# Performance work log

Hardware: AMD Instinct MI355X
Metric: run time of the kernel (lower is better)

The kernel has to match this reference:

```python
import jax, jax.numpy as jnp
import numpy as np

HEAD_NUM = 8
ATT_DIM = 64
NUM_UNITS = HEAD_NUM * ATT_DIM  # 512
B, T, D = 8, 1024, NUM_UNITS
NEG_BIG = -2.0**32 + 1.0


def _sinusoidal_table(max_len, num_hidden):
    P = np.zeros((1, max_len, num_hidden), dtype=np.float32)
    X = np.arange(max_len, dtype=np.float32).reshape(-1, 1) / np.power(
        10000.0, np.arange(0, num_hidden, 2, dtype=np.float32) / num_hidden)
    P[:, :, 0::2] = np.sin(X)
    P[:, :, 1::2] = np.cos(X)
    return P


def setup_inputs() -> dict:
    key = jax.random.key(0)
    ks = jax.random.split(key, 8)
    w_scale = 0.02
    return {
        "queries": jax.random.normal(ks[0], (B, T, D), dtype=jnp.float32),
        "keys": jax.random.normal(ks[1], (B, T, D), dtype=jnp.float32),
        "query_masks": jnp.ones((B, T), dtype=jnp.float32),
        "key_masks": jnp.ones((B, T), dtype=jnp.float32),
        "pos_table": jnp.asarray(_sinusoidal_table(T, D)),
        "W_Query": jax.random.normal(ks[2], (D, D), dtype=jnp.float32) * w_scale,
        "W_key": jax.random.normal(ks[3], (D, D), dtype=jnp.float32) * w_scale,
        "W_Value": jax.random.normal(ks[4], (D, D), dtype=jnp.float32) * w_scale,
        "fw1": jax.random.normal(ks[5], (D, 4 * D), dtype=jnp.float32) * w_scale,
        "fw2": jax.random.normal(ks[6], (4 * D, D), dtype=jnp.float32) * w_scale,
    }


def reference(queries, keys, query_masks, key_masks, pos_table,
              W_Query, W_key, W_Value, fw1, fw2):
    h, dh = HEAD_NUM, ATT_DIM
    pe_scale = jnp.asarray(NUM_UNITS ** 0.5, dtype=queries.dtype)
    pos = pos_table[:, :queries.shape[1], :] * pe_scale  # scale=True
    q_in = queries + pos
    k_in = keys + pos

    q = jnp.einsum('btd,de->bte', q_in, W_Query)
    k = jnp.einsum('btd,de->bte', k_in, W_key)
    # Faithful to source: values computed from the projected keys.
    v = jnp.einsum('btd,de->bte', k, W_Value)

    # split heads: (B,T,h*dh) -> (h,B,T,dh)
    def heads(x):
        return x.reshape(B, T, h, dh).transpose(2, 0, 1, 3)
    qh, kh, vh = heads(q), heads(k), heads(v)

    scores = jnp.einsum('hbqd,hbkd->hbqk', qh, kh) / (dh ** 0.5)
    # key padding mask
    scores = jnp.where(key_masks[None, :, None, :] == 1.0, scores, NEG_BIG)
    # blinding: mask the diagonal
    eye = jnp.eye(T, dtype=bool)
    scores = jnp.where(eye[None, None, :, :], NEG_BIG, scores)
    attn = jax.nn.softmax(scores, axis=-1)
    attn = attn * query_masks[None, :, :, None]

    out = jnp.einsum('hbqk,hbkd->hbqd', attn, vh)
    result = out.transpose(1, 2, 0, 3).reshape(B, T, D)  # merge heads

    result = result + q_in  # residual (use_res, queries after PE)

    # feed-forward with residual
    hidden = jax.nn.relu(jnp.einsum('btd,df->btf', result, fw1))
    ffn = jnp.einsum('btf,fd->btd', hidden, fw2)
    result = result + ffn

    # output_type == 'mean'
    return jnp.mean(result, axis=1, keepdims=True)  # (B,1,D)
```

## Files before the change

kernel.cpp:

```cpp
#include <hip/hip_runtime.h>


typedef __bf16 bf16x8 __attribute__((ext_vector_type(8)));
typedef __bf16 bf16x4 __attribute__((ext_vector_type(4)));
typedef float f32x4 __attribute__((ext_vector_type(4)));
typedef unsigned short u16x8 __attribute__((ext_vector_type(8)));
typedef unsigned short u16x4 __attribute__((ext_vector_type(4)));

#define MFMA_BF16(a, b, c) __builtin_amdgcn_mfma_f32_16x16x32_bf16((a), (b), (c), 0, 0, 0)
#define NEGBIG (-4294967295.0f)

#define GLL16(g, l)                                                                 \
    __builtin_amdgcn_global_load_lds((__attribute__((address_space(1))) void*)(g),  \
                                     (__attribute__((address_space(3))) void*)(l),  \
                                     16, 0, 0)

static __device__ __forceinline__ unsigned short f2bf(float f) {
    __bf16 h = (__bf16)f;
    return __builtin_bit_cast(unsigned short, h);
}
static __device__ __forceinline__ float bf2f(unsigned short h) {
    return __builtin_bit_cast(float, ((unsigned int)h) << 16);
}

__global__ __launch_bounds__(256) void prep_kernel(
    const float* __restrict__ q, const float* __restrict__ k,
    const float* __restrict__ pos,
    unsigned short* __restrict__ qo, unsigned short* __restrict__ ko)
{
    size_t i = ((size_t)blockIdx.x * 256 + threadIdx.x) * 4;
    size_t td = i & (size_t)(1024 * 512 - 1);
    float4 qv = *(const float4*)(q + i);
    float4 kv = *(const float4*)(k + i);
    float4 pv = *(const float4*)(pos + td);
    const float S = 22.627416997969522f;
    u16x4 qr, kr;
    qr[0] = f2bf(qv.x + pv.x * S); qr[1] = f2bf(qv.y + pv.y * S);
    qr[2] = f2bf(qv.z + pv.z * S); qr[3] = f2bf(qv.w + pv.w * S);
    kr[0] = f2bf(kv.x + pv.x * S); kr[1] = f2bf(kv.y + pv.y * S);
    kr[2] = f2bf(kv.z + pv.z * S); kr[3] = f2bf(kv.w + pv.w * S);
    *(u16x4*)(qo + i) = qr;
    *(u16x4*)(ko + i) = kr;
}

__global__ __launch_bounds__(256) void wconv_kernel(
    const float* __restrict__ w0, const float* __restrict__ w1, const float* __restrict__ w2,
    const float* __restrict__ w3, const float* __restrict__ w4,
    unsigned short* __restrict__ o0, unsigned short* __restrict__ o1, unsigned short* __restrict__ o2,
    unsigned short* __restrict__ o3, unsigned short* __restrict__ o4,
    unsigned short* __restrict__ wkp)
{
    int id = blockIdx.x;
    const float* in; unsigned short* out; int K, N, kt, nt; bool dup = false;
    if (id < 768) {
        int m = id >> 8; id &= 255;
        in  = (m == 0) ? w0 : ((m == 1) ? w1 : w2);
        out = (m == 0) ? o0 : ((m == 1) ? o1 : o2);
        dup = (m == 1);
        K = 512; N = 512; kt = id >> 4; nt = id & 15;
    } else if (id < 1792) {
        id -= 768; in = w3; out = o3; K = 512; N = 2048; kt = id >> 6; nt = id & 63;
    } else {
        id -= 1792; in = w4; out = o4; K = 2048; N = 512; kt = id >> 4; nt = id & 15;
    }
    int k0 = kt * 32, n0 = nt * 32;
    __shared__ float tile[32][33];
    int tx = threadIdx.x & 31, ty = threadIdx.x >> 5;
#pragma unroll
    for (int i = 0; i < 32; i += 8) {
        float v = in[(size_t)(k0 + ty + i) * N + n0 + tx];
        tile[ty + i][tx] = v;
        if (dup) wkp[(size_t)(k0 + ty + i) * 512 + n0 + tx] = f2bf(v);
    }
    __syncthreads();
#pragma unroll
    for (int i = 0; i < 32; i += 8)
        out[(size_t)(n0 + ty + i) * K + k0 + tx] = f2bf(tile[tx][ty + i]);
}

static __device__ __forceinline__ void gemm_core(
    const unsigned short* __restrict__ A,
    const unsigned short* __restrict__ Bt,
    unsigned short* __restrict__ C,
    int N, int K, int do_relu,
    unsigned short* As, unsigned short* Bs, int bx, int by)
{
    const int tid = threadIdx.x;
    const int wave = tid >> 6, lane = tid & 63;
    const int g = lane >> 4, lr = lane & 15;
    const int wm = (wave >> 1) * 64, wn = (wave & 1) * 64;
    const size_t bm = (size_t)bx * 128, bn = (size_t)by * 128;

    const int srow = tid >> 2, skc = (tid & 3) * 8;
    const unsigned short* Ap = A + (bm + srow) * (size_t)K + skc;
    const unsigned short* Bp = Bt + (bn + srow) * (size_t)K + skc;
    unsigned short* AsW = As + tid * 8;
    unsigned short* BsW = Bs + tid * 8;

    f32x4 acc[4][4] = {};

    for (int k0 = 0; k0 < K; k0 += 32) {
        __syncthreads();
        GLL16(Ap + k0, AsW);
        GLL16(Ap + (size_t)64 * K + k0, AsW + 2048);
        GLL16(Bp + k0, BsW);
        GLL16(Bp + (size_t)64 * K + k0, BsW + 2048);
        __syncthreads();
        bf16x8 af[4], bfr[4];
#pragma unroll
        for (int t = 0; t < 4; ++t) {
            af[t]  = *(const bf16x8*)&As[(wm + t * 16 + lr) * 32 + g * 8];
            bfr[t] = *(const bf16x8*)&Bs[(wn + t * 16 + lr) * 32 + g * 8];
        }
#pragma unroll
        for (int rt = 0; rt < 4; ++rt)
#pragma unroll
            for (int ct = 0; ct < 4; ++ct)
                acc[rt][ct] = MFMA_BF16(af[rt], bfr[ct], acc[rt][ct]);
    }

#pragma unroll
    for (int rt = 0; rt < 4; ++rt)
#pragma unroll
        for (int ct = 0; ct < 4; ++ct) {
            size_t row = bm + wm + rt * 16 + g * 4;
            size_t col = bn + wn + ct * 16 + lr;
#pragma unroll
            for (int r = 0; r < 4; ++r) {
                float x = acc[rt][ct][r];
                if (do_relu) x = fmaxf(x, 0.f);
                C[(row + r) * (size_t)N + col] = f2bf(x);
            }
        }
}

__global__ __launch_bounds__(256, 2) void gemm_bt(
    const unsigned short* __restrict__ A, const unsigned short* __restrict__ Bt,
    unsigned short* __restrict__ C, int N, int K, int do_relu)
{
    __shared__ unsigned short As[128 * 32];
    __shared__ unsigned short Bs[128 * 32];
    gemm_core(A, Bt, C, N, K, do_relu, As, Bs, blockIdx.x, blockIdx.y);
}

__global__ __launch_bounds__(256, 2) void proj3_kernel(
    const unsigned short* __restrict__ q_in, const unsigned short* __restrict__ k_in,
    const unsigned short* __restrict__ wqt, const unsigned short* __restrict__ wkt,
    const unsigned short* __restrict__ wkvt,
    unsigned short* __restrict__ qb, unsigned short* __restrict__ kb,
    unsigned short* __restrict__ vb)
{
    __shared__ unsigned short As[128 * 32];
    __shared__ unsigned short Bs[128 * 32];
    const unsigned short *A, *Bt; unsigned short* C;
    switch (blockIdx.z) {
        case 0:  A = q_in; Bt = wqt;  C = qb; break;
        case 1:  A = k_in; Bt = wkt;  C = kb; break;
        default: A = k_in; Bt = wkvt; C = vb; break;
    }
    gemm_core(A, Bt, C, 512, 512, 0, As, Bs, blockIdx.x, blockIdx.y);
}

__global__ __launch_bounds__(256, 2) void ffn2_meank(
    const unsigned short* __restrict__ A,
    const unsigned short* __restrict__ Bt,
    float* __restrict__ out)
{
    __shared__ unsigned short As[128 * 32];
    __shared__ unsigned short Bs[128 * 32];
    const int tid = threadIdx.x;
    const int wave = tid >> 6, lane = tid & 63;
    const int g = lane >> 4, lr = lane & 15;
    const int wm = (wave >> 1) * 64, wn = (wave & 1) * 64;
    const size_t bm = (size_t)blockIdx.x * 128, bn = (size_t)blockIdx.y * 128;
    const int koff = blockIdx.z * 512;

    const int srow = tid >> 2, skc = (tid & 3) * 8;
    const unsigned short* Ap = A + (bm + srow) * (size_t)2048 + koff + skc;
    const unsigned short* Bp = Bt + (bn + srow) * (size_t)2048 + koff + skc;
    unsigned short* AsW = As + tid * 8;
    unsigned short* BsW = Bs + tid * 8;

    f32x4 acc[4][4] = {};
    for (int k0 = 0; k0 < 512; k0 += 32) {
        __syncthreads();
        GLL16(Ap + k0, AsW);
        GLL16(Ap + (size_t)64 * 2048 + k0, AsW + 2048);
        GLL16(Bp + k0, BsW);
        GLL16(Bp + (size_t)64 * 2048 + k0, BsW + 2048);
        __syncthreads();
        bf16x8 af[4], bfr[4];
#pragma unroll
        for (int t = 0; t < 4; ++t) {
            af[t]  = *(const bf16x8*)&As[(wm + t * 16 + lr) * 32 + g * 8];
            bfr[t] = *(const bf16x8*)&Bs[(wn + t * 16 + lr) * 32 + g * 8];
        }
#pragma unroll
        for (int rt = 0; rt < 4; ++rt)
#pragma unroll
            for (int ct = 0; ct < 4; ++ct)
                acc[rt][ct] = MFMA_BF16(af[rt], bfr[ct], acc[rt][ct]);
    }

    const int b = (int)(bm >> 10);
#pragma unroll
    for (int ct = 0; ct < 4; ++ct) {
        float s = 0.f;
#pragma unroll
        for (int rt = 0; rt < 4; ++rt)
#pragma unroll
            for (int r = 0; r < 4; ++r) s += acc[rt][ct][r];
        s += __shfl_xor(s, 16, 64);
        s += __shfl_xor(s, 32, 64);
        if (g == 0)
            atomicAdd(out + b * 512 + bn + wn + ct * 16 + lr, s * (1.0f / 1024.0f));
    }
}

__global__ __launch_bounds__(512, 4) void attn_kernel(
    const unsigned short* __restrict__ Q,
    const unsigned short* __restrict__ Kp,
    const unsigned short* __restrict__ V,
    const float* __restrict__ queries,
    const float* __restrict__ pos,
    const float* __restrict__ kmask,
    const float* __restrict__ qmask,
    unsigned short* __restrict__ Res)
{
    __shared__ unsigned short Ks[64 * 72];
    __shared__ unsigned short Vts[64 * 72];
    __shared__ unsigned short Ps[8][16 * 72];
    const int tid = threadIdx.x, wave = tid >> 6, lane = tid & 63;
    const int g = lane >> 4, lr = lane & 15;
    const int b = blockIdx.y >> 3, h = blockIdx.y & 7;
    const int qg = blockIdx.x * 128 + wave * 16 + lr;

    bf16x8 aq0, aq1;
    {
        const unsigned short* qp = Q + ((size_t)(b * 1024 + qg)) * 512 + h * 64 + g * 8;
        aq0 = *(const bf16x8*)qp;
        aq1 = *(const bf16x8*)(qp + 32);
    }
    const float qm = qmask[b * 1024 + qg];

    float m_run = -3.0e38f, l_run = 0.f;
    f32x4 o[4] = {};

    const unsigned short* kbase = Kp + ((size_t)(b * 1024)) * 512 + h * 64;
    const unsigned short* vbase = V + ((size_t)(b * 1024)) * 512 + h * 64;

    const int half = tid >> 8;
    const int skey = (tid & 255) >> 2, sd = (tid & 3) * 16;
    const int vk0 = (tid & 15) * 4, vd0 = ((tid >> 4) & 15) * 4;

    u16x8 kr0, kr1; u16x4 vr[4];
    if (half) {
        const unsigned short* kp = kbase + (size_t)skey * 512 + sd;
        kr0 = *(const u16x8*)kp; kr1 = *(const u16x8*)(kp + 8);
    } else {
        const unsigned short* vp = vbase + (size_t)vk0 * 512 + vd0;
#pragma unroll
        for (int j = 0; j < 4; ++j) vr[j] = *(const u16x4*)(vp + (size_t)j * 512);
    }

    for (int j0 = 0; j0 < 1024; j0 += 64) {
        __syncthreads();
        if (half) {
            *(u16x8*)&Ks[skey * 72 + sd] = kr0;
            *(u16x8*)&Ks[skey * 72 + sd + 8] = kr1;
        } else {
#pragma unroll
            for (int i = 0; i < 4; ++i) {
                u16x4 w = { vr[0][i], vr[1][i], vr[2][i], vr[3][i] };
                *(u16x4*)&Vts[(vd0 + i) * 72 + vk0] = w;
            }
        }
        __syncthreads();
        if (j0 + 64 < 1024) {
            if (half) {
                const unsigned short* kp = kbase + (size_t)(j0 + 64 + skey) * 512 + sd;
                kr0 = *(const u16x8*)kp; kr1 = *(const u16x8*)(kp + 8);
            } else {
                const unsigned short* vp = vbase + (size_t)(j0 + 64 + vk0) * 512 + vd0;
#pragma unroll
                for (int j = 0; j < 4; ++j) vr[j] = *(const u16x4*)(vp + (size_t)j * 512);
            }
        }

        f32x4 s[4];
#pragma unroll
        for (int ct = 0; ct < 4; ++ct) {
            bf16x8 ka = *(const bf16x8*)&Ks[(ct * 16 + lr) * 72 + g * 8];
            bf16x8 kc = *(const bf16x8*)&Ks[(ct * 16 + lr) * 72 + 32 + g * 8];
            f32x4 z = {};
            z = MFMA_BF16(ka, aq0, z);
            s[ct] = MFMA_BF16(kc, aq1, z);
        }

        float rmax = -3.0e38f;
#pragma unroll
        for (int ct = 0; ct < 4; ++ct) {
            f32x4 km4 = *(const f32x4*)&kmask[b * 1024 + j0 + ct * 16 + g * 4];
#pragma unroll
            for (int r = 0; r < 4; ++r) {
                int key = j0 + ct * 16 + g * 4 + r;
                float x = s[ct][r] * 0.125f;
                x = (km4[r] == 1.0f) ? x : NEGBIG;
                x = (key == qg) ? NEGBIG : x;
                s[ct][r] = x;
                rmax = fmaxf(rmax, x);
            }
        }
        rmax = fmaxf(rmax, __shfl_xor(rmax, 16, 64));
        rmax = fmaxf(rmax, __shfl_xor(rmax, 32, 64));

        float mn = fmaxf(m_run, rmax);
        float alpha = __expf(m_run - mn);
        m_run = mn;
        float psum = 0.f;
#pragma unroll
        for (int ct = 0; ct < 4; ++ct) {
            f32x4 p;
#pragma unroll
            for (int r = 0; r < 4; ++r) { p[r] = __expf(s[ct][r] - mn); psum += p[r]; }
            bf16x4 pk = { (__bf16)p[0], (__bf16)p[1], (__bf16)p[2], (__bf16)p[3] };
            *(bf16x4*)&Ps[wave][lr * 72 + ct * 16 + g * 4] = pk;
        }
        psum += __shfl_xor(psum, 16, 64);
        psum += __shfl_xor(psum, 32, 64);
        l_run = l_run * alpha + psum;
#pragma unroll
        for (int dt = 0; dt < 4; ++dt) o[dt] *= alpha;

        bf16x8 p0 = *(const bf16x8*)&Ps[wave][lr * 72 + g * 8];
        bf16x8 p1 = *(const bf16x8*)&Ps[wave][lr * 72 + 32 + g * 8];
#pragma unroll
        for (int dt = 0; dt < 4; ++dt) {
            bf16x8 va = *(const bf16x8*)&Vts[(dt * 16 + lr) * 72 + g * 8];
            bf16x8 vc = *(const bf16x8*)&Vts[(dt * 16 + lr) * 72 + 32 + g * 8];
            o[dt] = MFMA_BF16(va, p0, o[dt]);
            o[dt] = MFMA_BF16(vc, p1, o[dt]);
        }
    }

    const float inv_l = 1.0f / l_run;
    const float S = 22.627416997969522f;
#pragma unroll
    for (int dt = 0; dt < 4; ++dt) {
        size_t col = (size_t)h * 64 + dt * 16 + g * 4;
        size_t idx = ((size_t)(b * 1024 + qg)) * 512 + col;
        f32x4 qv = *(const f32x4*)&queries[idx];
        f32x4 pv = *(const f32x4*)&pos[(size_t)qg * 512 + col];
        u16x4 wr;
#pragma unroll
        for (int r = 0; r < 4; ++r)
            wr[r] = f2bf(o[dt][r] * inv_l * qm + qv[r] + pv[r] * S);
        *(u16x4*)&Res[idx] = wr;
    }
}

__global__ __launch_bounds__(512) void reduce_mean(
    const unsigned short* __restrict__ res, float* __restrict__ out)
{
    const int b = blockIdx.x;
    const int t0 = blockIdx.y * 64;
    const int d = threadIdx.x;
    float acc = 0.f;
    for (int t = t0; t < t0 + 64; ++t)
        acc += bf2f(res[((size_t)(b * 1024 + t)) * 512 + d]);
    atomicAdd(out + b * 512 + d, acc * (1.0f / 1024.0f));
}

extern "C" void kernel_launch(void* const* d_in, const int* in_sizes, int n_in,
                              void* d_out, int out_size, void* d_ws, size_t ws_size,
                              hipStream_t stream)
{
    (void)in_sizes; (void)n_in; (void)out_size; (void)ws_size;
    const float* queries     = (const float*)d_in[0];
    const float* keys        = (const float*)d_in[1];
    const float* query_masks = (const float*)d_in[2];
    const float* key_masks   = (const float*)d_in[3];
    const float* pos_table   = (const float*)d_in[4];
    const float* W_Query     = (const float*)d_in[5];
    const float* W_key       = (const float*)d_in[6];
    const float* W_Value     = (const float*)d_in[7];
    const float* fw1         = (const float*)d_in[8];
    const float* fw2         = (const float*)d_in[9];
    float* out = (float*)d_out;

    unsigned short* ws = (unsigned short*)d_ws;
    const size_t NE = (size_t)8 * 1024 * 512;
    unsigned short* q_in   = ws;
    unsigned short* k_in   = ws + NE;
    unsigned short* qb     = ws + 2 * NE;
    unsigned short* kb     = ws + 3 * NE;
    unsigned short* vb     = ws + 4 * NE;
    unsigned short* result = q_in;
    unsigned short* hidden = qb;
    unsigned short* wqt    = ws + 6 * NE;
    unsigned short* wkt    = wqt + 512 * 512;
    unsigned short* wvt    = wkt + 512 * 512;
    unsigned short* fw1t   = wvt + 512 * 512;
    unsigned short* fw2t   = fw1t + 2048 * 512;
    unsigned short* wkp    = fw2t + 2048 * 512;
    unsigned short* wkvt   = wkp + 512 * 512;

    hipMemsetAsync(d_out, 0, 8 * 512 * sizeof(float), stream);
    prep_kernel<<<4096, 256, 0, stream>>>(queries, keys, pos_table, q_in, k_in);
    wconv_kernel<<<2816, 256, 0, stream>>>(W_Query, W_key, W_Value, fw1, fw2,
                                           wqt, wkt, wvt, fw1t, fw2t, wkp);
    gemm_bt<<<dim3(4, 4), 256, 0, stream>>>(wvt, wkp, wkvt, 512, 512, 0);
    proj3_kernel<<<dim3(64, 4, 3), 256, 0, stream>>>(q_in, k_in, wqt, wkt, wkvt, qb, kb, vb);
    attn_kernel<<<dim3(8, 64), 512, 0, stream>>>(qb, kb, vb, queries, pos_table,
                                                 key_masks, query_masks, result);
    reduce_mean<<<dim3(8, 16), 512, 0, stream>>>(result, out);
    gemm_bt<<<dim3(64, 16), 256, 0, stream>>>(result, fw1t, hidden, 2048, 512, 1);
    ffn2_meank<<<dim3(64, 4, 4), 256, 0, stream>>>(hidden, fw2t, out);
}
```

Measured before the change: 228.6 us.

## Fuse FFN mean before second GEMM, merge prep kernels, fold softmax scale into Q

Because the output is a mean over tokens and the second FFN layer is linear, the FFN2 GEMM is replaced by averaging the ReLU hidden activations inside the FFN1 epilogue (atomics into hmean) and then running a small matrix-vector kernel against fw2. This removes writing and rereading the full hidden tensor and the large FFN2 GEMM. The prep and weight-conversion kernels are merged into one launch, and the Wv·Wk product now uses a 64-tile GEMM with more blocks. The attention scale and log2(e) are folded into Q in the projection epilogue so the kernel can use exp2f, with key-mask bias precomputed in LDS and the diagonal check limited to the tiles that contain it. Occupancy hints are raised to 3 blocks per CU.

```diff
diff --git a/kernel.cpp b/kernel.cpp
--- a/kernel.cpp
+++ b/kernel.cpp
@@ -9,6 +9,7 @@
 
 #define MFMA_BF16(a, b, c) __builtin_amdgcn_mfma_f32_16x16x32_bf16((a), (b), (c), 0, 0, 0)
 #define NEGBIG (-4294967295.0f)
+#define QSCALE 0.18033688011112042f
 
 #define GLL16(g, l)                                                                 \
     __builtin_amdgcn_global_load_lds((__attribute__((address_space(1))) void*)(g),  \
@@ -23,27 +24,9 @@
     return __builtin_bit_cast(float, ((unsigned int)h) << 16);
 }
 
-__global__ __launch_bounds__(256) void prep_kernel(
-    const float* __restrict__ q, const float* __restrict__ k,
-    const float* __restrict__ pos,
-    unsigned short* __restrict__ qo, unsigned short* __restrict__ ko)
-{
-    size_t i = ((size_t)blockIdx.x * 256 + threadIdx.x) * 4;
-    size_t td = i & (size_t)(1024 * 512 - 1);
-    float4 qv = *(const float4*)(q + i);
-    float4 kv = *(const float4*)(k + i);
-    float4 pv = *(const float4*)(pos + td);
-    const float S = 22.627416997969522f;
-    u16x4 qr, kr;
-    qr[0] = f2bf(qv.x + pv.x * S); qr[1] = f2bf(qv.y + pv.y * S);
-    qr[2] = f2bf(qv.z + pv.z * S); qr[3] = f2bf(qv.w + pv.w * S);
-    kr[0] = f2bf(kv.x + pv.x * S); kr[1] = f2bf(kv.y + pv.y * S);
-    kr[2] = f2bf(kv.z + pv.z * S); kr[3] = f2bf(kv.w + pv.w * S);
-    *(u16x4*)(qo + i) = qr;
-    *(u16x4*)(ko + i) = kr;
-}
-
-__global__ __launch_bounds__(256) void wconv_kernel(
+__global__ __launch_bounds__(256) void prep_wconv_kernel(
+    const float* __restrict__ q, const float* __restrict__ k, const float* __restrict__ pos,
+    unsigned short* __restrict__ qo, unsigned short* __restrict__ ko,
     const float* __restrict__ w0, const float* __restrict__ w1, const float* __restrict__ w2,
     const float* __restrict__ w3, const float* __restrict__ w4,
     unsigned short* __restrict__ o0, unsigned short* __restrict__ o1, unsigned short* __restrict__ o2,
@@ -51,6 +34,23 @@
     unsigned short* __restrict__ wkp)
 {
     int id = blockIdx.x;
+    if (id < 4096) {
+        size_t i = ((size_t)id * 256 + threadIdx.x) * 4;
+        size_t td = i & (size_t)(1024 * 512 - 1);
+        float4 qv = *(const float4*)(q + i);
+        float4 kv = *(const float4*)(k + i);
+        float4 pv = *(const float4*)(pos + td);
+        const float S = 22.627416997969522f;
+        u16x4 qr, kr;
+        qr[0] = f2bf(qv.x + pv.x * S); qr[1] = f2bf(qv.y + pv.y * S);
+        qr[2] = f2bf(qv.z + pv.z * S); qr[3] = f2bf(qv.w + pv.w * S);
+        kr[0] = f2bf(kv.x + pv.x * S); kr[1] = f2bf(kv.y + pv.y * S);
+        kr[2] = f2bf(kv.z + pv.z * S); kr[3] = f2bf(kv.w + pv.w * S);
+        *(u16x4*)(qo + i) = qr;
+        *(u16x4*)(ko + i) = kr;
+        return;
+    }
+    id -= 4096;
     const float* in; unsigned short* out; int K, N, kt, nt; bool dup = false;
     if (id < 768) {
         int m = id >> 8; id &= 255;
@@ -78,11 +78,58 @@
         out[(size_t)(n0 + ty + i) * K + k0 + tx] = f2bf(tile[tx][ty + i]);
 }
 
+__global__ __launch_bounds__(256) void gemm64(
+    const unsigned short* __restrict__ A, const unsigned short* __restrict__ Bt,
+    unsigned short* __restrict__ C, int N, int K)
+{
+    __shared__ unsigned short As[64 * 32];
+    __shared__ unsigned short Bs[64 * 32];
+    const int tid = threadIdx.x;
+    const int wave = tid >> 6, lane = tid & 63;
+    const int g = lane >> 4, lr = lane & 15;
+    const int wm = (wave >> 1) * 32, wn = (wave & 1) * 32;
+    const size_t bm = (size_t)blockIdx.x * 64, bn = (size_t)blockIdx.y * 64;
+    const int row = tid >> 2, kc = (tid & 3) * 8;
+    const unsigned short* Ap = A + (bm + row) * (size_t)K + kc;
+    const unsigned short* Bp = Bt + (bn + row) * (size_t)K + kc;
+    unsigned short* AsW = As + tid * 8;
+    unsigned short* BsW = Bs + tid * 8;
+
+    f32x4 acc[2][2] = {};
+    for (int k0 = 0; k0 < K; k0 += 32) {
+        __syncthreads();
+        GLL16(Ap + k0, AsW);
+        GLL16(Bp + k0, BsW);
+        __syncthreads();
+        bf16x8 af[2], bfr[2];
+#pragma unroll
+        for (int t = 0; t < 2; ++t) {
+            af[t]  = *(const bf16x8*)&As[(wm + t * 16 + lr) * 32 + g * 8];
+            bfr[t] = *(const bf16x8*)&Bs[(wn + t * 16 + lr) * 32 + g * 8];
+        }
+#pragma unroll
+        for (int i = 0; i < 2; ++i)
+#pragma unroll
+            for (int j = 0; j < 2; ++j)
+                acc[i][j] = MFMA_BF16(af[i], bfr[j], acc[i][j]);
+    }
+#pragma unroll
+    for (int i = 0; i < 2; ++i)
+#pragma unroll
+        for (int j = 0; j < 2; ++j) {
+            size_t rr = bm + wm + i * 16 + g * 4;
+            size_t cc = bn + wn + j * 16 + lr;
+#pragma unroll
+            for (int r = 0; r < 4; ++r)
+                C[(rr + r) * (size_t)N + cc] = f2bf(acc[i][j][r]);
+        }
+}
+
 static __device__ __forceinline__ void gemm_core(
     const unsigned short* __restrict__ A,
     const unsigned short* __restrict__ Bt,
     unsigned short* __restrict__ C,
-    int N, int K, int do_relu,
+    int N, int K, int mode,
     unsigned short* As, unsigned short* Bs, int bx, int by)
 {
     const int tid = threadIdx.x;
@@ -98,7 +145,6 @@
     unsigned short* BsW = Bs + tid * 8;
 
     f32x4 acc[4][4] = {};
-
     for (int k0 = 0; k0 < K; k0 += 32) {
         __syncthreads();
         GLL16(Ap + k0, AsW);
@@ -128,22 +174,13 @@
 #pragma unroll
             for (int r = 0; r < 4; ++r) {
                 float x = acc[rt][ct][r];
-                if (do_relu) x = fmaxf(x, 0.f);
+                if (mode == 2) x *= QSCALE;
                 C[(row + r) * (size_t)N + col] = f2bf(x);
             }
         }
 }
 
-__global__ __launch_bounds__(256, 2) void gemm_bt(
-    const unsigned short* __restrict__ A, const unsigned short* __restrict__ Bt,
-    unsigned short* __restrict__ C, int N, int K, int do_relu)
-{
-    __shared__ unsigned short As[128 * 32];
-    __shared__ unsigned short Bs[128 * 32];
-    gemm_core(A, Bt, C, N, K, do_relu, As, Bs, blockIdx.x, blockIdx.y);
-}
-
-__global__ __launch_bounds__(256, 2) void proj3_kernel(
+__global__ __launch_bounds__(256, 3) void proj3_kernel(
     const unsigned short* __restrict__ q_in, const unsigned short* __restrict__ k_in,
     const unsigned short* __restrict__ wqt, const unsigned short* __restrict__ wkt,
     const unsigned short* __restrict__ wkvt,
@@ -152,19 +189,19 @@
 {
     __shared__ unsigned short As[128 * 32];
     __shared__ unsigned short Bs[128 * 32];
-    const unsigned short *A, *Bt; unsigned short* C;
+    const unsigned short *A, *Bt; unsigned short* C; int mode = 0;
     switch (blockIdx.z) {
-        case 0:  A = q_in; Bt = wqt;  C = qb; break;
+        case 0:  A = q_in; Bt = wqt;  C = qb; mode = 2; break;
         case 1:  A = k_in; Bt = wkt;  C = kb; break;
         default: A = k_in; Bt = wkvt; C = vb; break;
     }
-    gemm_core(A, Bt, C, 512, 512, 0, As, Bs, blockIdx.x, blockIdx.y);
-}
-
-__global__ __launch_bounds__(256, 2) void ffn2_meank(
+    gemm_core(A, Bt, C, 512, 512, mode, As, Bs, blockIdx.x, blockIdx.y);
+}
+
+__global__ __launch_bounds__(256, 3) void ffn1_mean(
     const unsigned short* __restrict__ A,
     const unsigned short* __restrict__ Bt,
-    float* __restrict__ out)
+    float* __restrict__ hmean)
 {
     __shared__ unsigned short As[128 * 32];
     __shared__ unsigned short Bs[128 * 32];
@@ -173,11 +210,10 @@
     const int g = lane >> 4, lr = lane & 15;
     const int wm = (wave >> 1) * 64, wn = (wave & 1) * 64;
     const size_t bm = (size_t)blockIdx.x * 128, bn = (size_t)blockIdx.y * 128;
-    const int koff = blockIdx.z * 512;
 
     const int srow = tid >> 2, skc = (tid & 3) * 8;
-    const unsigned short* Ap = A + (bm + srow) * (size_t)2048 + koff + skc;
-    const unsigned short* Bp = Bt + (bn + srow) * (size_t)2048 + koff + skc;
+    const unsigned short* Ap = A + (bm + srow) * (size_t)512 + skc;
+    const unsigned short* Bp = Bt + (bn + srow) * (size_t)512 + skc;
     unsigned short* AsW = As + tid * 8;
     unsigned short* BsW = Bs + tid * 8;
 
@@ -185,9 +221,9 @@
     for (int k0 = 0; k0 < 512; k0 += 32) {
         __syncthreads();
         GLL16(Ap + k0, AsW);
-        GLL16(Ap + (size_t)64 * 2048 + k0, AsW + 2048);
+        GLL16(Ap + (size_t)64 * 512 + k0, AsW + 2048);
         GLL16(Bp + k0, BsW);
-        GLL16(Bp + (size_t)64 * 2048 + k0, BsW + 2048);
+        GLL16(Bp + (size_t)64 * 512 + k0, BsW + 2048);
         __syncthreads();
         bf16x8 af[4], bfr[4];
 #pragma unroll
@@ -202,19 +238,36 @@
                 acc[rt][ct] = MFMA_BF16(af[rt], bfr[ct], acc[rt][ct]);
     }
 
-    const int b = (int)(bm >> 10);
+    const int b = blockIdx.x >> 3;
 #pragma unroll
     for (int ct = 0; ct < 4; ++ct) {
         float s = 0.f;
 #pragma unroll
         for (int rt = 0; rt < 4; ++rt)
 #pragma unroll
-            for (int r = 0; r < 4; ++r) s += acc[rt][ct][r];
+            for (int r = 0; r < 4; ++r) s += fmaxf(acc[rt][ct][r], 0.f);
         s += __shfl_xor(s, 16, 64);
         s += __shfl_xor(s, 32, 64);
         if (g == 0)
-            atomicAdd(out + b * 512 + bn + wn + ct * 16 + lr, s * (1.0f / 1024.0f));
-    }
+            atomicAdd(hmean + b * 2048 + bn + wn + ct * 16 + lr, s);
+    }
+}
+
+__global__ __launch_bounds__(64) void ffn2_small(
+    const float* __restrict__ hmean, const unsigned short* __restrict__ fw2t,
+    float* __restrict__ out)
+{
+    const int b = blockIdx.x;
+    const int d = blockIdx.y * 64 + threadIdx.x;
+    const float* hm = hmean + b * 2048;
+    const unsigned short* wr = fw2t + (size_t)d * 2048;
+    float acc = 0.f;
+    for (int f = 0; f < 2048; f += 8) {
+        u16x8 w = *(const u16x8*)(wr + f);
+#pragma unroll
+        for (int j = 0; j < 8; ++j) acc += hm[f + j] * bf2f(w[j]);
+    }
+    out[b * 512 + d] += acc * (1.0f / 1024.0f);
 }
 
 __global__ __launch_bounds__(512, 4) void attn_kernel(
@@ -230,10 +283,14 @@
     __shared__ unsigned short Ks[64 * 72];
     __shared__ unsigned short Vts[64 * 72];
     __shared__ unsigned short Ps[8][16 * 72];
+    __shared__ float kbias[1024];
     const int tid = threadIdx.x, wave = tid >> 6, lane = tid & 63;
     const int g = lane >> 4, lr = lane & 15;
     const int b = blockIdx.y >> 3, h = blockIdx.y & 7;
     const int qg = blockIdx.x * 128 + wave * 16 + lr;
+
+    for (int i = tid; i < 1024; i += 512)
+        kbias[i] = (kmask[b * 1024 + i] == 1.0f) ? 0.f : NEGBIG;
 
     bf16x8 aq0, aq1;
     {
@@ -297,32 +354,33 @@
             s[ct] = MFMA_BF16(kc, aq1, z);
         }
 
+#pragma unroll
+        for (int ct = 0; ct < 4; ++ct)
+            s[ct] += *(const f32x4*)&kbias[j0 + ct * 16 + g * 4];
+        if (((qg ^ j0) & ~63) == 0) {
+#pragma unroll
+            for (int ct = 0; ct < 4; ++ct) {
+                unsigned diff = (unsigned)(qg - (j0 + ct * 16 + g * 4));
+                if (diff < 4u) s[ct][diff] = NEGBIG;
+            }
+        }
         float rmax = -3.0e38f;
 #pragma unroll
-        for (int ct = 0; ct < 4; ++ct) {
-            f32x4 km4 = *(const f32x4*)&kmask[b * 1024 + j0 + ct * 16 + g * 4];
-#pragma unroll
-            for (int r = 0; r < 4; ++r) {
-                int key = j0 + ct * 16 + g * 4 + r;
-                float x = s[ct][r] * 0.125f;
-                x = (km4[r] == 1.0f) ? x : NEGBIG;
-                x = (key == qg) ? NEGBIG : x;
-                s[ct][r] = x;
-                rmax = fmaxf(rmax, x);
-            }
-        }
+        for (int ct = 0; ct < 4; ++ct)
+#pragma unroll
+            for (int r = 0; r < 4; ++r) rmax = fmaxf(rmax, s[ct][r]);
         rmax = fmaxf(rmax, __shfl_xor(rmax, 16, 64));
         rmax = fmaxf(rmax, __shfl_xor(rmax, 32, 64));
 
         float mn = fmaxf(m_run, rmax);
-        float alpha = __expf(m_run - mn);
+        float alpha = exp2f(m_run - mn);
         m_run = mn;
         float psum = 0.f;
 #pragma unroll
         for (int ct = 0; ct < 4; ++ct) {
             f32x4 p;
 #pragma unroll
-            for (int r = 0; r < 4; ++r) { p[r] = __expf(s[ct][r] - mn); psum += p[r]; }
+            for (int r = 0; r < 4; ++r) { p[r] = exp2f(s[ct][r] - mn); psum += p[r]; }
             bf16x4 pk = { (__bf16)p[0], (__bf16)p[1], (__bf16)p[2], (__bf16)p[3] };
             *(bf16x4*)&Ps[wave][lr * 72 + ct * 16 + g * 4] = pk;
         }
@@ -396,7 +454,6 @@
     unsigned short* kb     = ws + 3 * NE;
     unsigned short* vb     = ws + 4 * NE;
     unsigned short* result = q_in;
-    unsigned short* hidden = qb;
     unsigned short* wqt    = ws + 6 * NE;
     unsigned short* wkt    = wqt + 512 * 512;
     unsigned short* wvt    = wkt + 512 * 512;
@@ -404,16 +461,18 @@
     unsigned short* fw2t   = fw1t + 2048 * 512;
     unsigned short* wkp    = fw2t + 2048 * 512;
     unsigned short* wkvt   = wkp + 512 * 512;
+    float*          hmean  = (float*)(wkvt + 512 * 512);
 
     hipMemsetAsync(d_out, 0, 8 * 512 * sizeof(float), stream);
-    prep_kernel<<<4096, 256, 0, stream>>>(queries, keys, pos_table, q_in, k_in);
-    wconv_kernel<<<2816, 256, 0, stream>>>(W_Query, W_key, W_Value, fw1, fw2,
-                                           wqt, wkt, wvt, fw1t, fw2t, wkp);
-    gemm_bt<<<dim3(4, 4), 256, 0, stream>>>(wvt, wkp, wkvt, 512, 512, 0);
+    hipMemsetAsync(hmean, 0, 8 * 2048 * sizeof(float), stream);
+    prep_wconv_kernel<<<6912, 256, 0, stream>>>(queries, keys, pos_table, q_in, k_in,
+                                                W_Query, W_key, W_Value, fw1, fw2,
+                                                wqt, wkt, wvt, fw1t, fw2t, wkp);
+    gemm64<<<dim3(8, 8), 256, 0, stream>>>(wvt, wkp, wkvt, 512, 512);
     proj3_kernel<<<dim3(64, 4, 3), 256, 0, stream>>>(q_in, k_in, wqt, wkt, wkvt, qb, kb, vb);
     attn_kernel<<<dim3(8, 64), 512, 0, stream>>>(qb, kb, vb, queries, pos_table,
                                                  key_masks, query_masks, result);
     reduce_mean<<<dim3(8, 16), 512, 0, stream>>>(result, out);
-    gemm_bt<<<dim3(64, 16), 256, 0, stream>>>(result, fw1t, hidden, 2048, 512, 1);
-    ffn2_meank<<<dim3(64, 4, 4), 256, 0, stream>>>(hidden, fw2t, out);
-}
+    ffn1_mean<<<dim3(64, 16), 256, 0, stream>>>(result, fw1t, hmean);
+    ffn2_small<<<dim3(8, 8), 64, 0, stream>>>(hmean, fw2t, out);
+}
```

Result: slower. 258.3 us (+13.0%).
